# Performance work log

Measured on AMD Instinct MI355X. Metric: run time of the kernel, lower is better.

## Reference

```python
import jax, jax.numpy as jnp
import numpy as np

B, T, D = 2, 2048, 2048
H, HD = 16, 128            # num_heads, head_dim = D // H
DVH = 2                    # dynamic_value_num_heads
NVK = 4                    # num_v_keys = int(sqrt(H))
TOPK = DVH * 2             # = 4 <= NVK


def setup_inputs() -> dict:
    key = jax.random.key(0)
    ks = jax.random.split(key, 12)
    s = jnp.float32(0.02)
    return {
        "x": jax.random.normal(ks[0], (B, T, D), jnp.float32),
        "Wq": jax.random.normal(ks[1], (D, D), jnp.float32) * s,
        "bq": jnp.zeros((D,), jnp.float32),
        "Wk": jax.random.normal(ks[2], (D, D), jnp.float32) * s,
        "bk": jnp.zeros((D,), jnp.float32),
        "Wvq": jax.random.normal(ks[3], (HD * DVH, D), jnp.float32) * s,
        "bvq": jnp.zeros((HD * DVH,), jnp.float32),
        "v_keys": jax.random.normal(ks[4], (DVH, NVK, HD), jnp.float32) * s,
        "v_embed": jax.random.normal(ks[5], (H, HD * H), jnp.float32) * s,
        "Wo": jax.random.normal(ks[6], (D, D), jnp.float32) * s,
        "bo": jnp.zeros((D,), jnp.float32),
    }


def reference(x, Wq, bq, Wk, bk, Wvq, bvq, v_keys, v_embed, Wo, bo):
    b, t, d = x.shape
    # q/k projections -> [b, H, t, HD]
    q = (x @ Wq.T + bq).reshape(b, t, H, HD).transpose(0, 2, 1, 3)
    k = (x @ Wk.T + bk).reshape(b, t, H, HD).transpose(0, 2, 1, 3)

    # --- compute_value_states ---
    vq = (x @ Wvq.T + bvq).reshape(b, t, DVH, HD)          # [b,t,h,n]
    sim = jnp.einsum('bthn,hkn->bthk', vq, v_keys)         # [b,t,DVH,NVK]
    _, idx = jax.lax.top_k(sim, TOPK)                      # [b,t,DVH,TOPK]
    ve = v_embed[idx]                                      # gather -> [b,t,DVH,TOPK,d]
    # einsum 'btd,bthkd->btd' == x * sum over (h,k)
    vs = x * ve.sum(axis=(2, 3))                           # [b,t,d]
    v = vs.reshape(b, t, H, HD).transpose(0, 2, 1, 3)      # [b,H,t,HD]

    # --- hand-rolled causal attention ---
    scores = jnp.einsum('bhqd,bhkd->bhqk', q, k) / np.float32(np.sqrt(HD))
    min_val = jnp.finfo(x.dtype).min
    mask = jnp.triu(jnp.full((t, t), min_val, dtype=x.dtype), 1)
    scores = scores + mask
    w = jax.nn.softmax(scores.astype(jnp.float32), axis=-1).astype(x.dtype)
    o = jnp.einsum('bhqk,bhkd->bhqd', w, v)                # [b,H,t,HD]
    o = o.transpose(0, 2, 1, 3).reshape(b, t, d)
    return o @ Wo.T + bo
```

## Files before the change

kernel.cpp:

```cpp
#include <hip/hip_runtime.h>
#include <hip/hip_bf16.h>

#define DEV __device__ __forceinline__

typedef __bf16 bf16x8 __attribute__((ext_vector_type(8)));
typedef __bf16 bf16x4 __attribute__((ext_vector_type(4)));
typedef float f32x4 __attribute__((ext_vector_type(4)));

static constexpr int kB = 2, kT = 2048, kD = 2048, kH = 16, kHD = 128;
static constexpr int kBT = kB * kT;

#if __has_builtin(__builtin_amdgcn_exp2f)
DEV float fast_exp2(float x) { return __builtin_amdgcn_exp2f(x); }
#else
DEV float fast_exp2(float x) { return exp2f(x); }
#endif

DEV unsigned short f2bf(float f) {
  union { __hip_bfloat16 h; unsigned short u; } cv;
  cv.h = __float2bfloat16(f);
  return cv.u;
}

DEV void gl_lds16(const void* g, void* l) {
  __builtin_amdgcn_global_load_lds(
      (const __attribute__((address_space(1))) unsigned int*)g,
      (__attribute__((address_space(3))) unsigned int*)l, 16, 0, 0);
}

#define MFMA(a, b, c) __builtin_amdgcn_mfma_f32_16x16x32_bf16(a, b, c, 0, 0, 0)

DEV int swz4(int row) { return (row ^ (row >> 2)) & 3; }

__global__ __launch_bounds__(256) void cvt4_kernel(
    const float* __restrict__ s0, const float* __restrict__ s1,
    const float* __restrict__ s2, const float* __restrict__ s3,
    unsigned short* __restrict__ d0, unsigned short* __restrict__ d1,
    unsigned short* __restrict__ d2, unsigned short* __restrict__ d3,
    int n0, int n1) {
  const int y = blockIdx.y;
  const float* s = y == 0 ? s0 : y == 1 ? s1 : y == 2 ? s2 : s3;
  unsigned short* d = y == 0 ? d0 : y == 1 ? d1 : y == 2 ? d2 : d3;
  const int n4 = y == 0 ? n0 : n1;
  int i = blockIdx.x * 256 + threadIdx.x;
  if (i >= n4) return;
  float4 v = ((const float4*)s)[i];
  ushort4 o;
  o.x = f2bf(v.x); o.y = f2bf(v.y); o.z = f2bf(v.z); o.w = f2bf(v.w);
  ((ushort4*)d)[i] = o;
}

__global__ __launch_bounds__(256) void make_vt_kernel(
    const float* __restrict__ x, const float* __restrict__ v_embed,
    unsigned short* __restrict__ vt) {
  __shared__ __align__(16) unsigned short sT[128 * 72];
  const int t0 = blockIdx.x * 64, h = blockIdx.y, b = blockIdx.z;
  const int tid = threadIdx.x;
  const int d4 = tid & 31, r8 = tid >> 5;
  const int dg = h * kHD + d4 * 4;
  float4 e0 = *(const float4*)(v_embed + dg);
  float4 e1 = *(const float4*)(v_embed + kD + dg);
  float4 e2 = *(const float4*)(v_embed + 2 * kD + dg);
  float4 e3 = *(const float4*)(v_embed + 3 * kD + dg);
  float4 c4;
  c4.x = 2.f * (e0.x + e1.x + e2.x + e3.x);
  c4.y = 2.f * (e0.y + e1.y + e2.y + e3.y);
  c4.z = 2.f * (e0.z + e1.z + e2.z + e3.z);
  c4.w = 2.f * (e0.w + e1.w + e2.w + e3.w);
#pragma unroll
  for (int it = 0; it < 8; it++) {
    const int t = r8 + it * 8;
    float4 v = *(const float4*)(x + (size_t)(b * kT + t0 + t) * kD + dg);
    sT[(d4 * 4 + 0) * 72 + t] = f2bf(v.x * c4.x);
    sT[(d4 * 4 + 1) * 72 + t] = f2bf(v.y * c4.y);
    sT[(d4 * 4 + 2) * 72 + t] = f2bf(v.z * c4.z);
    sT[(d4 * 4 + 3) * 72 + t] = f2bf(v.w * c4.w);
  }
  __syncthreads();
#pragma unroll
  for (int it = 0; it < 4; it++) {
    const int hd = (tid >> 3) + it * 32;
    const int tt = (tid & 7) * 8;
    bf16x8 vv = *(const bf16x8*)(sT + hd * 72 + tt);
    *(bf16x8*)(vt + ((size_t)((b * kH + h) * kHD + hd)) * kT + t0 + tt) = vv;
  }
}

template <bool BF16OUT, bool FUSED2>
__global__ __launch_bounds__(256, 4) void gemm_bt(
    const unsigned short* __restrict__ A, const unsigned short* __restrict__ B1,
    const unsigned short* __restrict__ B2, const float* __restrict__ bias1,
    const float* __restrict__ bias2, void* __restrict__ C1, void* __restrict__ C2,
    float scale1, float scale2) {
  constexpr int N = kD, K = kD;
  __shared__ __align__(16) unsigned short As[128 * 32], Bs[128 * 32];
  const unsigned short* Bm = (FUSED2 && blockIdx.z) ? B2 : B1;
  const float* bias = (FUSED2 && blockIdx.z) ? bias2 : bias1;
  void* Cout = (FUSED2 && blockIdx.z) ? C2 : C1;
  const float scale = (FUSED2 && blockIdx.z) ? scale2 : scale1;
  const int tid = threadIdx.x;
  const int lane = tid & 63, wave = tid >> 6;
  const int wr = wave >> 1, wc = wave & 1;
  const int m0 = blockIdx.y * 128, n0 = blockIdx.x * 128;
  const int frow = lane & 15, fc = lane >> 4;

  f32x4 acc[4][4];
  for (int i = 0; i < 4; i++)
    for (int j = 0; j < 4; j++)
      for (int r = 0; r < 4; r++) acc[i][j][r] = 0.f;

  const int r0 = tid >> 2, c0 = (tid & 3) ^ swz4(r0);
  const int p1 = tid + 256;
  const int r1 = p1 >> 2, c1 = (p1 & 3) ^ swz4(r1);

  const unsigned short* Ab = A + (size_t)m0 * K;
  const unsigned short* Bb = Bm + (size_t)n0 * K;

  for (int k0 = 0; k0 < K; k0 += 32) {
    __syncthreads();
    gl_lds16(Ab + (size_t)r0 * K + k0 + c0 * 8, As + tid * 8);
    gl_lds16(Ab + (size_t)r1 * K + k0 + c1 * 8, As + p1 * 8);
    gl_lds16(Bb + (size_t)r0 * K + k0 + c0 * 8, Bs + tid * 8);
    gl_lds16(Bb + (size_t)r1 * K + k0 + c1 * 8, Bs + p1 * 8);
    __syncthreads();
    bf16x8 af[4], bfr[4];
    for (int mi = 0; mi < 4; mi++) {
      int row = wr * 64 + mi * 16 + frow;
      af[mi] = *(const bf16x8*)(As + (row * 4 + (fc ^ swz4(row))) * 8);
    }
    for (int ni = 0; ni < 4; ni++) {
      int row = wc * 64 + ni * 16 + frow;
      bfr[ni] = *(const bf16x8*)(Bs + (row * 4 + (fc ^ swz4(row))) * 8);
    }
    for (int mi = 0; mi < 4; mi++)
      for (int ni = 0; ni < 4; ni++)
        acc[mi][ni] = MFMA(af[mi], bfr[ni], acc[mi][ni]);
  }
  for (int ni = 0; ni < 4; ni++) {
    const int n = n0 + wc * 64 + ni * 16 + frow;
    const float bs = bias[n];
    for (int mi = 0; mi < 4; mi++) {
      const int mb = m0 + wr * 64 + mi * 16 + fc * 4;
      for (int r = 0; r < 4; r++) {
        const float v = (acc[mi][ni][r] + bs) * scale;
        if (BF16OUT)
          ((unsigned short*)Cout)[(size_t)(mb + r) * N + n] = f2bf(v);
        else
          ((float*)Cout)[(size_t)(mb + r) * N + n] = v;
      }
    }
  }
}

__global__ __launch_bounds__(256, 2) void attn2_kernel(
    const unsigned short* __restrict__ Q, const unsigned short* __restrict__ Kg,
    const unsigned short* __restrict__ Vt, unsigned short* __restrict__ O) {
  __shared__ __align__(16) unsigned short sK[2][64 * 128];
  __shared__ __align__(16) unsigned short sV[2][64 * 128];
  const int tid = threadIdx.x, l = tid & 63, w = tid >> 6;
  const int g = l >> 4, q15 = l & 15;
  const int bid = blockIdx.x;
  const int xcd = bid & 7, rest = bid >> 3;
  const int gidx = xcd + 8 * (rest & 3);
  const int pi = rest >> 2;
  const int h = gidx & 15, b = gidx >> 4;

  for (int half = 0; half < 2; half++) {
    const int qt = half == 0 ? (31 - pi) : pi;
    const int q0 = qt * 64;
    const int nkb = qt + 1;
    const int q = q0 + w * 16 + q15;

    __syncthreads();
    for (int i = 0; i < 4; i++) {
      const int idx = tid + i * 256;
      const int key = idx >> 4, cc = (idx & 15) ^ (key & 15);
      gl_lds16(Kg + (size_t)(b * kT + key) * kD + h * kHD + cc * 8,
               &sK[0][idx * 8]);
    }
    for (int i = 0; i < 4; i++) {
      const int idx = tid + i * 256;
      const int hd = idx >> 3;
      const int cc = (idx & 7) ^ (hd & 7) ^ (((hd >> 3) & 1) << 2);
      gl_lds16(Vt + ((size_t)((b * kH + h) * kHD + hd)) * kT + cc * 8,
               &sV[0][idx * 8]);
    }

    bf16x8 qf[4];
    const unsigned short* Qrow = Q + (size_t)(b * kT + q) * kD + h * kHD;
#pragma unroll
    for (int kk = 0; kk < 4; kk++)
      qf[kk] = *(const bf16x8*)(Qrow + kk * 32 + g * 8);

    f32x4 oacc[8];
#pragma unroll
    for (int ni = 0; ni < 8; ni++)
      for (int r = 0; r < 4; r++) oacc[ni][r] = 0.f;
    float m_i = -1e30f, l_i = 0.f;

    for (int kb = 0; kb < nkb; kb++) {
      const int bb = kb & 1;
      __syncthreads();
      if (kb + 1 < nkb) {
        const int k0n = (kb + 1) * 64;
        const int nb = 1 - bb;
#pragma unroll
        for (int i = 0; i < 4; i++) {
          const int idx = tid + i * 256;
          const int key = idx >> 4, cc = (idx & 15) ^ (key & 15);
          gl_lds16(Kg + (size_t)(b * kT + k0n + key) * kD + h * kHD + cc * 8,
                   &sK[nb][idx * 8]);
        }
#pragma unroll
        for (int i = 0; i < 4; i++) {
          const int idx = tid + i * 256;
          const int hd = idx >> 3;
          const int cc = (idx & 7) ^ (hd & 7) ^ (((hd >> 3) & 1) << 2);
          gl_lds16(Vt + ((size_t)((b * kH + h) * kHD + hd)) * kT + k0n + cc * 8,
                   &sV[nb][idx * 8]);
        }
      }

      f32x4 st[4];
#pragma unroll
      for (int s = 0; s < 4; s++)
        for (int r = 0; r < 4; r++) st[s][r] = 0.f;
#pragma unroll
      for (int s = 0; s < 4; s++) {
        const int key = s * 16 + q15;
#pragma unroll
        for (int kk = 0; kk < 4; kk++) {
          bf16x8 kf = *(const bf16x8*)(
              &sK[bb][(key * 16 + ((kk * 4 + g) ^ (key & 15))) * 8]);
          st[s] = MFMA(kf, qf[kk], st[s]);
        }
      }
      if (kb == nkb - 1) {
        const int k0 = kb * 64;
#pragma unroll
        for (int s = 0; s < 4; s++)
          for (int r = 0; r < 4; r++)
            if (k0 + s * 16 + g * 4 + r > q) st[s][r] = -1e30f;
      }
      float mx = -1e30f;
#pragma unroll
      for (int s = 0; s < 4; s++)
        for (int r = 0; r < 4; r++) mx = fmaxf(mx, st[s][r]);
      mx = fmaxf(mx, __shfl_xor(mx, 16, 64));
      mx = fmaxf(mx, __shfl_xor(mx, 32, 64));
      const float mn = fmaxf(m_i, mx);
      const float alpha = fast_exp2(m_i - mn);
      float rs = 0.f;
      union { bf16x8 v; unsigned short u[8]; } pkv[2];
#pragma unroll
      for (int s = 0; s < 4; s++)
        for (int r = 0; r < 4; r++) {
          const float p = fast_exp2(st[s][r] - mn);
          rs += p;
          pkv[s >> 1].u[(s & 1) * 4 + r] = f2bf(p);
        }
      rs += __shfl_xor(rs, 16, 64);
      rs += __shfl_xor(rs, 32, 64);
      m_i = mn;
      l_i = l_i * alpha + rs;
#pragma unroll
      for (int ni = 0; ni < 8; ni++)
        for (int r = 0; r < 4; r++) oacc[ni][r] *= alpha;
#pragma unroll
      for (int ni = 0; ni < 8; ni++) {
        const int hd = ni * 16 + q15;
        const int hx = (hd & 7) ^ (((hd >> 3) & 1) << 2), base = hd * 8;
#pragma unroll
        for (int c = 0; c < 2; c++) {
          const int c4l = 8 * c + g;
          const int c4h = 8 * c + 4 + g;
          bf16x4 lo = *(const bf16x4*)(
              &sV[bb][(base + ((c4l >> 1) ^ hx)) * 8 + (c4l & 1) * 4]);
          bf16x4 hi = *(const bf16x4*)(
              &sV[bb][(base + ((c4h >> 1) ^ hx)) * 8 + (c4h & 1) * 4]);
          bf16x8 vf = __builtin_shufflevector(lo, hi, 0, 1, 2, 3, 4, 5, 6, 7);
          oacc[ni] = MFMA(vf, pkv[c].v, oacc[ni]);
        }
      }
    }
    const float inv = 1.f / l_i;
    unsigned short* Orow = O + (size_t)(b * kT + q) * kD + h * kHD;
#pragma unroll
    for (int ni = 0; ni < 8; ni++) {
      ushort4 o4;
      o4.x = f2bf(oacc[ni][0] * inv);
      o4.y = f2bf(oacc[ni][1] * inv);
      o4.z = f2bf(oacc[ni][2] * inv);
      o4.w = f2bf(oacc[ni][3] * inv);
      *(ushort4*)(Orow + ni * 16 + g * 4) = o4;
    }
  }
}

extern "C" void kernel_launch(void* const* d_in, const int* in_sizes, int n_in,
                              void* d_out, int out_size, void* d_ws, size_t ws_size,
                              hipStream_t stream) {
  const float* x       = (const float*)d_in[0];
  const float* Wq      = (const float*)d_in[1];
  const float* bq      = (const float*)d_in[2];
  const float* Wk      = (const float*)d_in[3];
  const float* bk      = (const float*)d_in[4];
  const float* v_embed = (const float*)d_in[8];
  const float* Wo      = (const float*)d_in[9];
  const float* bo      = (const float*)d_in[10];
  float* out = (float*)d_out;

  char* w = (char*)d_ws;
  unsigned short* xb  = (unsigned short*)w; w += (size_t)kBT * kD * 2;
  unsigned short* qb  = (unsigned short*)w; w += (size_t)kBT * kD * 2;
  unsigned short* kb  = (unsigned short*)w; w += (size_t)kBT * kD * 2;
  unsigned short* ob  = (unsigned short*)w; w += (size_t)kBT * kD * 2;
  unsigned short* vtb = (unsigned short*)w; w += (size_t)kBT * kD * 2;
  unsigned short* wqb = (unsigned short*)w; w += (size_t)kD * kD * 2;
  unsigned short* wkb = (unsigned short*)w; w += (size_t)kD * kD * 2;
  unsigned short* wob = (unsigned short*)w; w += (size_t)kD * kD * 2;

  cvt4_kernel<<<dim3(kBT * kD / 1024, 4), 256, 0, stream>>>(
      x, Wq, Wk, Wo, xb, wqb, wkb, wob, kBT * kD / 4, kD * kD / 4);
  make_vt_kernel<<<dim3(kT / 64, kH, kB), 256, 0, stream>>>(x, v_embed, vtb);

  const float scaleQ = 0.08838834764831845f * 1.4426950408889634f;
  gemm_bt<true, true><<<dim3(kD / 128, kBT / 128, 2), 256, 0, stream>>>(
      xb, wqb, wkb, bq, bk, qb, kb, scaleQ, 1.0f);

  attn2_kernel<<<dim3(512), 256, 0, stream>>>(qb, kb, vtb, ob);

  gemm_bt<false, false><<<dim3(kD / 128, kBT / 128, 1), 256, 0, stream>>>(
      ob, wob, nullptr, bo, nullptr, out, nullptr, 1.0f, 1.0f);
}
```

Baseline: 339.8 us.

## Replace GEMM with 256-wide tiles and triple-buffered async LDS pipeline

```diff
diff --git a/kernel.cpp b/kernel.cpp
--- a/kernel.cpp
+++ b/kernel.cpp
@@ -86,61 +86,143 @@
   }
 }
 
-template <bool BF16OUT, bool FUSED2>
-__global__ __launch_bounds__(256, 4) void gemm_bt(
+template <int MREP, bool BF16OUT, bool FUSED2>
+__global__ __launch_bounds__(512, 2) void gemm256(
     const unsigned short* __restrict__ A, const unsigned short* __restrict__ B1,
     const unsigned short* __restrict__ B2, const float* __restrict__ bias1,
     const float* __restrict__ bias2, void* __restrict__ C1, void* __restrict__ C2,
     float scale1, float scale2) {
+  constexpr int BM = MREP * 32;
   constexpr int N = kD, K = kD;
-  __shared__ __align__(16) unsigned short As[128 * 32], Bs[128 * 32];
+  constexpr int NT = K / 32;
+  constexpr int ALOADS = MREP / 4;
+  __shared__ __align__(16) unsigned short As[3][BM * 32];
+  __shared__ __align__(16) unsigned short Bs[3][256 * 32];
   const unsigned short* Bm = (FUSED2 && blockIdx.z) ? B2 : B1;
   const float* bias = (FUSED2 && blockIdx.z) ? bias2 : bias1;
   void* Cout = (FUSED2 && blockIdx.z) ? C2 : C1;
   const float scale = (FUSED2 && blockIdx.z) ? scale2 : scale1;
   const int tid = threadIdx.x;
   const int lane = tid & 63, wave = tid >> 6;
-  const int wr = wave >> 1, wc = wave & 1;
-  const int m0 = blockIdx.y * 128, n0 = blockIdx.x * 128;
+  const int wr = wave >> 2, wc = wave & 3;
+  const int m0 = blockIdx.y * BM, n0 = blockIdx.x * 256;
   const int frow = lane & 15, fc = lane >> 4;
 
-  f32x4 acc[4][4];
-  for (int i = 0; i < 4; i++)
+  f32x4 acc[MREP][4];
+#pragma unroll
+  for (int i = 0; i < MREP; i++)
+#pragma unroll
     for (int j = 0; j < 4; j++)
+#pragma unroll
       for (int r = 0; r < 4; r++) acc[i][j][r] = 0.f;
-
-  const int r0 = tid >> 2, c0 = (tid & 3) ^ swz4(r0);
-  const int p1 = tid + 256;
-  const int r1 = p1 >> 2, c1 = (p1 & 3) ^ swz4(r1);
 
   const unsigned short* Ab = A + (size_t)m0 * K;
   const unsigned short* Bb = Bm + (size_t)n0 * K;
 
-  for (int k0 = 0; k0 < K; k0 += 32) {
-    __syncthreads();
-    gl_lds16(Ab + (size_t)r0 * K + k0 + c0 * 8, As + tid * 8);
-    gl_lds16(Ab + (size_t)r1 * K + k0 + c1 * 8, As + p1 * 8);
-    gl_lds16(Bb + (size_t)r0 * K + k0 + c0 * 8, Bs + tid * 8);
-    gl_lds16(Bb + (size_t)r1 * K + k0 + c1 * 8, Bs + p1 * 8);
-    __syncthreads();
-    bf16x8 af[4], bfr[4];
+  auto stageA = [&](int bf, int k0) {
+#pragma unroll
+    for (int i = 0; i < ALOADS; i++) {
+      const int p = tid + i * 512;
+      const int r = p >> 2, c = (p & 3) ^ swz4(r);
+      gl_lds16(Ab + (size_t)r * K + k0 + c * 8, &As[bf][p * 8]);
+    }
+  };
+  auto stageB = [&](int bf, int k0) {
+#pragma unroll
+    for (int i = 0; i < 2; i++) {
+      const int p = tid + i * 512;
+      const int r = p >> 2, c = (p & 3) ^ swz4(r);
+      gl_lds16(Bb + (size_t)r * K + k0 + c * 8, &Bs[bf][p * 8]);
+    }
+  };
+
+  stageA(0, 0); stageB(0, 0);
+  stageA(1, 32); stageB(1, 32);
+  if constexpr (MREP == 8)
+    asm volatile("s_waitcnt vmcnt(4)" ::: "memory");
+  else
+    asm volatile("s_waitcnt vmcnt(3)" ::: "memory");
+  __builtin_amdgcn_s_barrier();
+  __builtin_amdgcn_sched_barrier(0);
+
+  int buf = 0;
+  for (int t = 0; t < NT; t++) {
+    const int nbuf = buf == 0 ? 2 : buf - 1;
+    const int kn = (t + 2) * 32;
+    const bool pre = t + 2 < NT;
+    const unsigned short* Asb = As[buf];
+    const unsigned short* Bsb = Bs[buf];
+
+    bf16x8 bfr[4], af[4];
+#pragma unroll
+    for (int ni = 0; ni < 4; ni++) {
+      const int row = wc * 64 + ni * 16 + frow;
+      bfr[ni] = *(const bf16x8*)(Bsb + (row * 4 + (fc ^ swz4(row))) * 8);
+    }
+#pragma unroll
     for (int mi = 0; mi < 4; mi++) {
-      int row = wr * 64 + mi * 16 + frow;
-      af[mi] = *(const bf16x8*)(As + (row * 4 + (fc ^ swz4(row))) * 8);
-    }
-    for (int ni = 0; ni < 4; ni++) {
-      int row = wc * 64 + ni * 16 + frow;
-      bfr[ni] = *(const bf16x8*)(Bs + (row * 4 + (fc ^ swz4(row))) * 8);
-    }
+      const int row = wr * (MREP * 16) + mi * 16 + frow;
+      af[mi] = *(const bf16x8*)(Asb + (row * 4 + (fc ^ swz4(row))) * 8);
+    }
+    if (pre) stageA(nbuf, kn);
+    if constexpr (MREP == 4) {
+      if (pre) {
+        stageB(nbuf, kn);
+        asm volatile("s_waitcnt vmcnt(3)" ::: "memory");
+      } else if (t + 1 < NT) {
+        asm volatile("s_waitcnt vmcnt(0)" ::: "memory");
+      }
+    }
+    __builtin_amdgcn_s_barrier();
+    asm volatile("s_waitcnt lgkmcnt(0)" ::: "memory");
+    __builtin_amdgcn_sched_barrier(0);
+    __builtin_amdgcn_s_setprio(1);
+#pragma unroll
     for (int mi = 0; mi < 4; mi++)
+#pragma unroll
       for (int ni = 0; ni < 4; ni++)
         acc[mi][ni] = MFMA(af[mi], bfr[ni], acc[mi][ni]);
+    __builtin_amdgcn_s_setprio(0);
+    __builtin_amdgcn_s_barrier();
+    __builtin_amdgcn_sched_barrier(0);
+
+    if constexpr (MREP == 8) {
+      bf16x8 af2[4];
+#pragma unroll
+      for (int mi = 0; mi < 4; mi++) {
+        const int row = wr * 128 + (mi + 4) * 16 + frow;
+        af2[mi] = *(const bf16x8*)(Asb + (row * 4 + (fc ^ swz4(row))) * 8);
+      }
+      if (pre) {
+        stageB(nbuf, kn);
+        asm volatile("s_waitcnt vmcnt(4)" ::: "memory");
+      } else if (t + 1 < NT) {
+        asm volatile("s_waitcnt vmcnt(0)" ::: "memory");
+      }
+      __builtin_amdgcn_s_barrier();
+      asm volatile("s_waitcnt lgkmcnt(0)" ::: "memory");
+      __builtin_amdgcn_sched_barrier(0);
+      __builtin_amdgcn_s_setprio(1);
+#pragma unroll
+      for (int mi = 0; mi < 4; mi++)
+#pragma unroll
+        for (int ni = 0; ni < 4; ni++)
+          acc[mi + 4][ni] = MFMA(af2[mi], bfr[ni], acc[mi + 4][ni]);
+      __builtin_amdgcn_s_setprio(0);
+      __builtin_amdgcn_s_barrier();
+      __builtin_amdgcn_sched_barrier(0);
+    }
+    buf = buf == 2 ? 0 : buf + 1;
   }
+
+#pragma unroll
   for (int ni = 0; ni < 4; ni++) {
     const int n = n0 + wc * 64 + ni * 16 + frow;
     const float bs = bias[n];
-    for (int mi = 0; mi < 4; mi++) {
-      const int mb = m0 + wr * 64 + mi * 16 + fc * 4;
+#pragma unroll
+    for (int mi = 0; mi < MREP; mi++) {
+      const int mb = m0 + wr * (MREP * 16) + mi * 16 + fc * 4;
+#pragma unroll
       for (int r = 0; r < 4; r++) {
         const float v = (acc[mi][ni][r] + bs) * scale;
         if (BF16OUT)
@@ -325,11 +407,11 @@
   make_vt_kernel<<<dim3(kT / 64, kH, kB), 256, 0, stream>>>(x, v_embed, vtb);
 
   const float scaleQ = 0.08838834764831845f * 1.4426950408889634f;
-  gemm_bt<true, true><<<dim3(kD / 128, kBT / 128, 2), 256, 0, stream>>>(
+  gemm256<8, true, true><<<dim3(kD / 256, kBT / 256, 2), 512, 0, stream>>>(
       xb, wqb, wkb, bq, bk, qb, kb, scaleQ, 1.0f);
 
   attn2_kernel<<<dim3(512), 256, 0, stream>>>(qb, kb, vtb, ob);
 
-  gemm_bt<false, false><<<dim3(kD / 128, kBT / 128, 1), 256, 0, stream>>>(
+  gemm256<4, false, false><<<dim3(kD / 256, kBT / 128, 1), 512, 0, stream>>>(
       ob, wob, nullptr, bo, nullptr, out, nullptr, 1.0f, 1.0f);
 }
```

New measurement: 350.5 us. 1.03x slower.
